# Optimization experiments

Hardware: AMD Instinct MI355X
Metric: run time of the kernel (lower is better)

## Reference

```python
import jax, jax.numpy as jnp
import numpy as np

B, S, D = 8, 4096, 256
H, DK, DV = 8, 32, 32


def _layer_norm(x, g, b, eps=1e-6):
    mu = jnp.mean(x, axis=-1, keepdims=True)
    var = jnp.mean(jnp.square(x - mu), axis=-1, keepdims=True)
    return (x - mu) * jax.lax.rsqrt(var + eps) * g + b


def setup_inputs() -> dict:
    key = jax.random.key(0)
    ks = jax.random.split(key, 16)
    std = 1.0 / np.sqrt(D)
    p = lambda k, shp: (jax.random.normal(k, shp, jnp.float32) * std)
    return {
        "h": jax.random.normal(ks[0], (B, S, D), jnp.float32),
        "e": jax.random.normal(ks[1], (B, S, D), jnp.float32),
        "s": jax.random.normal(ks[2], (B, D), jnp.float32),
        "sat_wq": p(ks[3], (D, H * DK)), "sat_wk": p(ks[4], (D, H * DK)),
        "sat_wv": p(ks[5], (D, H * DV)), "sat_wo": p(ks[6], (H * DV, D)),
        "sat_g": jnp.ones((D,), jnp.float32), "sat_b": jnp.zeros((D,), jnp.float32),
        "rel_wq": p(ks[7], (D, H * DK)), "rel_wk": p(ks[8], (D, H * DK)),
        "rel_wv": p(ks[9], (D, H * DV)), "rel_wo": p(ks[10], (H * DV, D)),
        "rel_g": jnp.ones((D,), jnp.float32), "rel_b": jnp.zeros((D,), jnp.float32),
    }


def reference(h, e, s, sat_wq, sat_wk, sat_wv, sat_wo, sat_g, sat_b,
              rel_wq, rel_wk, rel_wv, rel_wo, rel_g, rel_b):
    b, sl, d = h.shape
    scale = 1.0 / np.sqrt(DK)

    # ---- build 5-token context: [left, self, right, entity, relay] ----
    hp = jnp.pad(h, ((0, 0), (1, 1), (0, 0)))  # zeros at both ends
    s_exp = jnp.broadcast_to(s[:, None, :], (b, sl, d))
    ctx = jnp.stack([hp[:, :sl], h, hp[:, 2:], e, s_exp], axis=2)  # [B,S,5,D]

    # ---- satellite attention: 1 query vs 5-token context per position ----
    q = (h @ sat_wq).reshape(b, sl, H, DK)
    k = (ctx @ sat_wk).reshape(b, sl, 5, H, DK)
    v = (ctx @ sat_wv).reshape(b, sl, 5, H, DV)
    attn = jax.nn.softmax(jnp.einsum('bshd,bschd->bshc', q, k) * scale, axis=-1)
    o = jnp.einsum('bshc,bschd->bshd', attn, v).reshape(b, sl, H * DV) @ sat_wo
    h_out = _layer_norm(o + h, sat_g, sat_b)  # [B,S,D]

    # ---- relay attention: relay query vs [s; h_out] ----
    s_h = jnp.concatenate([s[:, None, :], h_out], axis=1)  # [B,S+1,D]
    qr = (s @ rel_wq).reshape(b, H, DK)
    kr = (s_h @ rel_wk).reshape(b, sl + 1, H, DK)
    vr = (s_h @ rel_wv).reshape(b, sl + 1, H, DV)
    attn_r = jax.nn.softmax(jnp.einsum('bhd,bkhd->bhk', qr, kr) * scale, axis=-1)
    orl = jnp.einsum('bhk,bkhd->bhd', attn_r, vr).reshape(b, H * DV) @ rel_wo
    s_out = _layer_norm(orl + s, rel_g, rel_b)  # [B,D]

    return (h_out, s_out)
```

## Files before the change

### kernel.cpp

```cpp
#include <hip/hip_runtime.h>
#include <hip/hip_bf16.h>

typedef unsigned short ushort_t;
typedef unsigned int uint_t;
typedef __attribute__((ext_vector_type(8))) short bf16x8;
typedef __attribute__((ext_vector_type(4))) float f32x4;

#define NB 8
#define NS 4096
#define ND 256
#define NH 8
#define NDK 32
#define NBS (NB*NS)
#define NK  (NS+1)
#define CH  513
#define NCH 8
static const size_t PBUF = (size_t)NB*(NS+1)*ND;
static const size_t HSZ  = (size_t)NBS*ND;

__device__ __forceinline__ ushort_t f2b(float x){
  union { __hip_bfloat16 b; ushort_t u; } cv; cv.b = __float2bfloat16(x); return cv.u;
}
__device__ __forceinline__ float b2f(ushort_t u){
  union { uint_t u; float f; } cv; cv.u = ((uint_t)u) << 16; return cv.f;
}
__device__ __forceinline__ void gload16(const ushort_t* g, ushort_t* l){
  __builtin_amdgcn_global_load_lds(
      (const __attribute__((address_space(1))) void*)g,
      (__attribute__((address_space(3))) void*)l, 16, 0, 0);
}
__device__ __forceinline__ uint4 packbf16x8(float4 a, float4 b){
  uint4 p;
  p.x = f2b(a.x) | ((uint_t)f2b(a.y)<<16);
  p.y = f2b(a.z) | ((uint_t)f2b(a.w)<<16);
  p.z = f2b(b.x) | ((uint_t)f2b(b.y)<<16);
  p.w = f2b(b.z) | ((uint_t)f2b(b.w)<<16);
  return p;
}

__device__ __forceinline__ float bsum256(float v){
  __shared__ float tmp[4];
  #pragma unroll
  for (int o=32;o>0;o>>=1) v += __shfl_down(v,o);
  if ((threadIdx.x & 63)==0) tmp[threadIdx.x>>6] = v;
  __syncthreads();
  float r = tmp[0]+tmp[1]+tmp[2]+tmp[3];
  __syncthreads();
  return r;
}

__global__ __launch_bounds__(256) void prep(
    const float* __restrict__ w0, const float* __restrict__ w1, const float* __restrict__ w2,
    const float* __restrict__ w3, const float* __restrict__ w4, const float* __restrict__ w5,
    ushort_t* __restrict__ WtAll,
    const float* __restrict__ s,
    const float* __restrict__ rwq,
    ushort_t* __restrict__ ksb, ushort_t* __restrict__ vsb,
    float* __restrict__ qr, ushort_t* __restrict__ krv)
{
  __shared__ float sh[64*68];
  const int blk = blockIdx.x;
  const int tid = threadIdx.x;
  if (blk < 96){
    const int z = blk >> 4, xy = blk & 15;
    const float* W = (z==0)?w0:(z==1)?w1:(z==2)?w2:(z==3)?w3:(z==4)?w4:w5;
    ushort_t* Wt = WtAll + (size_t)z*65536;
    float (*t)[68] = (float(*)[68])sh;
    const int k0 = (xy>>2)*64, n0 = (xy&3)*64;
    const int tr = tid>>4, tc4 = (tid&15)*4;
    #pragma unroll
    for (int i=0;i<4;i++){
      int r = tr + i*16;
      float4 v = *(const float4*)&W[(size_t)(k0+r)*ND + n0 + tc4];
      t[r][tc4]=v.x; t[r][tc4+1]=v.y; t[r][tc4+2]=v.z; t[r][tc4+3]=v.w;
    }
    __syncthreads();
    #pragma unroll
    for (int i=0;i<4;i++){
      int n = tr + i*16;
      uint_t q0 = f2b(t[tc4+0][n]) | ((uint_t)f2b(t[tc4+1][n])<<16);
      uint_t q1 = f2b(t[tc4+2][n]) | ((uint_t)f2b(t[tc4+3][n])<<16);
      *(uint2*)&Wt[(size_t)(n0+n)*ND + k0 + tc4] = make_uint2(q0,q1);
    }
  } else {
    const int rem = blk - 96;
    const int b = rem & 7, which = rem >> 3;
    const float* W = (which==0)?w1:(which==1)?w2:(which==2)?rwq:(which==3)?w4:w5;
    float* a = sh;
    a[tid] = s[(size_t)b*ND + tid];
    __syncthreads();
    float acc = 0.f;
    #pragma unroll 8
    for (int d=0; d<ND; d++)
      acc = fmaf(a[d], W[(size_t)d*ND + tid], acc);
    switch (which){
      case 0: ksb[(size_t)b*ND + tid] = f2b(acc); break;
      case 1: vsb[(size_t)b*ND + tid] = f2b(acc); break;
      case 2: qr[(size_t)b*ND + tid] = acc; break;
      case 3: krv[(size_t)b*NK*512 + tid] = f2b(acc); break;
      default: krv[(size_t)b*NK*512 + 256 + tid] = f2b(acc); break;
    }
  }
}

__global__ __launch_bounds__(512) void gemm_qkve(const float* __restrict__ hA,
    const float* __restrict__ eA, const ushort_t* __restrict__ Wt,
    ushort_t* __restrict__ hQKV, ushort_t* __restrict__ eKV)
{
  __shared__ __align__(16) ushort_t Ap[64][256];
  __shared__ __align__(16) ushort_t Bs[3][128][64];
  const int blk = blockIdx.x;
  const bool isH = blk < 512;
  const float* A = isH ? hA : eA;
  const ushort_t* Wb = isH ? Wt : (Wt + 65536);
  ushort_t* Y = isH ? hQKV : eKV;
  const int ldn  = isH ? 768 : 512;
  const int ncol = isH ? 6 : 4;
  const int row0 = (blk & 511) * 64;
  const int tid = threadIdx.x;
  const int lane = tid & 63;
  const int wave = tid >> 6;
  const int wr  = (wave>>2)*32;
  const int wcw = (wave&3)*32;
  const int l15 = lane & 15, lg = lane >> 4;
  const int lr8 = lane >> 3;
  const int ls  = (lane & 7) ^ lr8;

  #pragma unroll
  for (int i=0;i<4;i++){
    int sgi = tid + i*512;
    int r   = sgi >> 5;
    int c8  = (sgi & 31) * 8;
    const float* ga = A + (size_t)(row0 + r)*ND + c8;
    float4 a0 = *(const float4*)ga, a1 = *(const float4*)(ga+4);
    int byte = r*512 + ((c8*2) ^ ((r&7)<<4));
    *(uint4*)((char*)&Ap[0][0] + byte) = packbf16x8(a0,a1);
  }
  asm volatile("s_waitcnt lgkmcnt(0)" ::: "memory");

  const ushort_t* Bbase = Wb + (size_t)(wave*16 + lr8)*ND + ls*8;
  #define STAGEB(ct, kt, bb) do{ \
    const ushort_t* bp = Bbase + (size_t)(ct)*128*ND + (kt)*64; \
    gload16(bp,                &Bs[bb][wave*16][0]); \
    gload16(bp + (size_t)8*ND, &Bs[bb][wave*16+8][0]); \
  }while(0)

  const f32x4 vzero = {0.f,0.f,0.f,0.f};
  f32x4 acc[2][2] = {};
  const int total = ncol*4;
  STAGEB(0, 0, 0);
  int bcur = 0, bnxt = 1;
  for (int s = 0; s < total; ++s){
    const int kt = s & 3;
    const bool more = (s+1 < total);
    if (more) STAGEB((s+1)>>2, (s+1)&3, bnxt);
    if (more) asm volatile("s_waitcnt vmcnt(2)" ::: "memory");
    else      asm volatile("s_waitcnt vmcnt(0)" ::: "memory");
    __builtin_amdgcn_s_barrier();
    __builtin_amdgcn_sched_barrier(0);
    #pragma unroll
    for (int ks=0; ks<2; ks++){
      bf16x8 af[2], bfr[2];
      #pragma unroll
      for (int mi=0;mi<2;mi++){
        int ra  = wr + mi*16 + l15;
        int cb2 = kt*128 + ks*64 + lg*16;
        af[mi] = *(const bf16x8*)((const char*)&Ap[0][0] + ra*512 + (cb2 ^ ((ra&7)<<4)));
      }
      #pragma unroll
      for (int ni=0;ni<2;ni++){
        int rb = wcw + ni*16 + l15;
        int cb = (ks<<6) + (lg<<4);
        bfr[ni] = *(const bf16x8*)((const char*)&Bs[bcur][0][0] + rb*128 + (cb ^ ((rb&7)<<4)));
      }
      #pragma unroll
      for (int mi=0;mi<2;mi++)
        #pragma unroll
        for (int ni=0;ni<2;ni++)
          acc[mi][ni] = __builtin_amdgcn_mfma_f32_16x16x32_bf16(af[mi], bfr[ni], acc[mi][ni], 0,0,0);
    }
    bcur = bnxt; bnxt = (bnxt == 2) ? 0 : bnxt + 1;
    if (kt == 3){
      const int col0 = (s >> 2) * 128;
      #pragma unroll
      for (int mi=0;mi<2;mi++)
        #pragma unroll
        for (int r=0;r<4;r++){
          size_t orow = (size_t)(row0 + wr + mi*16 + lg*4 + r);
          #pragma unroll
          for (int ni=0;ni<2;ni++)
            Y[orow*(size_t)ldn + col0 + wcw + ni*16 + l15] = f2b(acc[mi][ni][r]);
        }
      #pragma unroll
      for (int mi=0;mi<2;mi++)
        #pragma unroll
        for (int ni=0;ni<2;ni++)
          acc[mi][ni] = vzero;
    }
  }
  #undef STAGEB
}

__global__ __launch_bounds__(512) void oproj_krv(const ushort_t* __restrict__ A,
    const ushort_t* __restrict__ Wto, const ushort_t* __restrict__ WtKRV,
    const float* __restrict__ hres,
    const float* __restrict__ g, const float* __restrict__ bta,
    float* __restrict__ outf, ushort_t* __restrict__ krv)
{
  __shared__ __align__(16) ushort_t Pool[2][128][64];
  __shared__ __align__(16) ushort_t Ap[64][256];
  __shared__ float rs[64][4], rq[64][4];
  __shared__ float gl[ND], bl[ND];
  const int tid  = threadIdx.x;
  const int row0 = blockIdx.x*64;
  const int lane = tid & 63;
  const int wave = tid >> 6;
  const int wr = (wave>>2)*32;
  const int wc = (wave&3)*64;
  const int wcw = (wave&3)*32;
  const int l15 = lane & 15, lg = lane >> 4;
  const int lr8 = lane >> 3;
  const int ls  = (lane & 7) ^ lr8;

  if (tid < ND){ gl[tid] = g[tid]; bl[tid] = bta[tid]; }

  ushort_t (*As)[64][64] = (ushort_t(*)[64][64])&Pool[0][0][0];
  const ushort_t* Asrc = A + (size_t)(row0 + wave*8 + lr8)*ND + ls*8;

  f32x4 acc[2][4] = {};

  #define STAGE3(t, bb) gload16(Asrc + (t)*64, &As[bb][wave*8][0])
  #define COMPUTE3(t, bb) do{ \
    _Pragma("unroll") \
    for (int ks=0; ks<2; ks++){ \
      bf16x8 af[2], bfr[4]; \
      _Pragma("unroll") \
      for (int mi=0;mi<2;mi++){ \
        int ra = wr + mi*16 + l15; int cb = (ks<<6) + (lg<<4); \
        af[mi] = *(const bf16x8*)((const char*)&As[bb][0][0] + ra*128 + (cb ^ ((ra&7)<<4))); \
      } \
      _Pragma("unroll") \
      for (int ni=0;ni<4;ni++) \
        bfr[ni] = *(const bf16x8*)&Wto[(size_t)(wc + ni*16 + l15)*ND + (t)*64 + ks*32 + lg*8]; \
      _Pragma("unroll") \
      for (int mi=0;mi<2;mi++) \
        _Pragma("unroll") \
        for (int ni=0;ni<4;ni++) \
          acc[mi][ni] = __builtin_amdgcn_mfma_f32_16x16x32_bf16(af[mi], bfr[ni], acc[mi][ni], 0,0,0); \
    } \
  }while(0)

  STAGE3(0, 0);
  __syncthreads();
  STAGE3(1, 1); COMPUTE3(0, 0); __syncthreads();
  STAGE3(2, 0); COMPUTE3(1, 1); __syncthreads();
  STAGE3(3, 1); COMPUTE3(2, 0); __syncthreads();
  COMPUTE3(3, 1);
  #undef STAGE3
  #undef COMPUTE3

  #pragma unroll
  for (int mi=0;mi<2;mi++)
    #pragma unroll
    for (int rr=0;rr<4;rr++){
      size_t rowb = (size_t)(row0 + wr + mi*16 + lg*4 + rr)*ND;
      #pragma unroll
      for (int ni=0;ni<4;ni++)
        acc[mi][ni][rr] += hres[rowb + wc + ni*16 + l15];
    }

  #pragma unroll
  for (int mi=0;mi<2;mi++)
    #pragma unroll
    for (int rr=0;rr<4;rr++){
      float sv = 0.f, qv = 0.f;
      #pragma unroll
      for (int ni=0;ni<4;ni++){ float x = acc[mi][ni][rr]; sv += x; qv += x*x; }
      #pragma unroll
      for (int o=1;o<16;o<<=1){ sv += __shfl_xor(sv,o); qv += __shfl_xor(qv,o); }
      if (l15 == 0){
        int rl = wr + mi*16 + lg*4 + rr;
        rs[rl][wave&3] = sv; rq[rl][wave&3] = qv;
      }
    }
  __syncthreads();

  #pragma unroll
  for (int mi=0;mi<2;mi++)
    #pragma unroll
    for (int rr=0;rr<4;rr++){
      int rl = wr + mi*16 + lg*4 + rr;
      float sm = rs[rl][0] + rs[rl][1] + rs[rl][2] + rs[rl][3];
      float sq = rq[rl][0] + rq[rl][1] + rq[rl][2] + rq[rl][3];
      float mu = sm * (1.0f/ND);
      float var = sq * (1.0f/ND) - mu*mu;
      float rstd = rsqrtf(var + 1e-6f);
      size_t rowb = (size_t)(row0 + rl)*ND;
      #pragma unroll
      for (int ni=0;ni<4;ni++){
        int col = wc + ni*16 + l15;
        float yv = (acc[mi][ni][rr] - mu)*rstd*gl[col] + bl[col];
        outf[rowb + col] = yv;
        int byte = rl*512 + ((col*2) ^ ((rl&7)<<4));
        *(ushort_t*)((char*)&Ap[0][0] + byte) = f2b(yv);
      }
    }

  const ushort_t* Bbase = WtKRV + (size_t)(wave*16 + lr8)*ND + ls*8;
  #define STAGEB(ct, kt, bb) do{ \
    const ushort_t* bp = Bbase + (size_t)(ct)*128*ND + (kt)*64; \
    gload16(bp,                &Pool[bb][wave*16][0]); \
    gload16(bp + (size_t)8*ND, &Pool[bb][wave*16+8][0]); \
  }while(0)

  const f32x4 vzero = {0.f,0.f,0.f,0.f};
  f32x4 acc2[2][2] = {};
  STAGEB(0,0,0);
  __syncthreads();
  int buf = 0;
  for (int s = 0; s < 16; ++s){
    const int kt = s & 3;
    if (s+1 < 16) STAGEB((s+1)>>2, (s+1)&3, buf^1);
    #pragma unroll
    for (int ks=0; ks<2; ks++){
      bf16x8 af[2], bfr[2];
      #pragma unroll
      for (int mi=0;mi<2;mi++){
        int ra  = wr + mi*16 + l15;
        int cb2 = kt*128 + ks*64 + lg*16;
        af[mi] = *(const bf16x8*)((const char*)&Ap[0][0] + ra*512 + (cb2 ^ ((ra&7)<<4)));
      }
      #pragma unroll
      for (int ni=0;ni<2;ni++){
        int rb = wcw + ni*16 + l15;
        int cb = (ks<<6) + (lg<<4);
        bfr[ni] = *(const bf16x8*)((const char*)&Pool[buf][0][0] + rb*128 + (cb ^ ((rb&7)<<4)));
      }
      #pragma unroll
      for (int mi=0;mi<2;mi++)
        #pragma unroll
        for (int ni=0;ni<2;ni++)
          acc2[mi][ni] = __builtin_amdgcn_mfma_f32_16x16x32_bf16(af[mi], bfr[ni], acc2[mi][ni], 0,0,0);
    }
    __syncthreads();
    buf ^= 1;
    if (kt == 3){
      const int col0 = (s >> 2) * 128;
      #pragma unroll
      for (int mi=0;mi<2;mi++)
        #pragma unroll
        for (int r=0;r<4;r++){
          int row = row0 + wr + mi*16 + lg*4 + r;
          size_t orow = (size_t)(row>>12)*NK + 1 + (row&4095);
          #pragma unroll
          for (int ni=0;ni<2;ni++)
            krv[orow*512 + col0 + wcw + ni*16 + l15] = f2b(acc2[mi][ni][r]);
        }
      #pragma unroll
      for (int mi=0;mi<2;mi++)
        #pragma unroll
        for (int ni=0;ni<2;ni++)
          acc2[mi][ni] = vzero;
    }
  }
  #undef STAGEB
}

__device__ __forceinline__ void load8(float* d, const ushort_t* p){
  bf16x8 v = *(const bf16x8*)p;
  #pragma unroll
  for (int i=0;i<8;i++) d[i] = b2f((ushort_t)v[i]);
}
__device__ __forceinline__ void zero8(float* d){
  #pragma unroll
  for (int i=0;i<8;i++) d[i] = 0.f;
}
__global__ __launch_bounds__(256) void sat_attn4(const ushort_t* __restrict__ HQ,
    const ushort_t* __restrict__ EKV,
    const ushort_t* __restrict__ KS, const ushort_t* __restrict__ VS,
    ushort_t* __restrict__ O)
{
  const int tid = threadIdx.x;
  const int l  = tid & 3;
  const int g  = tid >> 2;
  const int hh = g & 7;
  const int pi = g >> 3;
  const int pos = blockIdx.x*8 + pi;
  const int b = pos >> 12, t = pos & 4095;
  const int co = hh*NDK + l*8;
  const float scale = 0.17677669529663687f;

  const size_t rq = (size_t)pos*768;
  const size_t re = (size_t)pos*512;
  float q[8], k0[8], k1[8], k2[8], k3[8], k4[8];
  load8(q,  HQ + rq + co);
  load8(k1, HQ + rq + 256 + co);
  load8(k3, EKV + re + co);
  load8(k4, KS + (size_t)b*ND + co);
  if (t > 0)    load8(k0, HQ + rq - 768 + 256 + co);
  else          zero8(k0);
  if (t < NS-1) load8(k2, HQ + rq + 768 + 256 + co);
  else          zero8(k2);

  float s0=0.f,s1=0.f,s2=0.f,s3=0.f,s4=0.f;
  #pragma unroll
  for (int i=0;i<8;i++){
    s0 = fmaf(q[i],k0[i],s0); s1 = fmaf(q[i],k1[i],s1); s2 = fmaf(q[i],k2[i],s2);
    s3 = fmaf(q[i],k3[i],s3); s4 = fmaf(q[i],k4[i],s4);
  }
  #pragma unroll
  for (int mm=1; mm<4; mm<<=1){
    s0 += __shfl_xor(s0,mm); s1 += __shfl_xor(s1,mm); s2 += __shfl_xor(s2,mm);
    s3 += __shfl_xor(s3,mm); s4 += __shfl_xor(s4,mm);
  }
  s0*=scale; s1*=scale; s2*=scale; s3*=scale; s4*=scale;
  float m = fmaxf(fmaxf(fmaxf(s0,s1),fmaxf(s2,s3)),s4);
  float p0=expf(s0-m), p1=expf(s1-m), p2=expf(s2-m), p3=expf(s3-m), p4=expf(s4-m);
  float inv = 1.0f/(p0+p1+p2+p3+p4);

  float v0[8], v1[8], v2[8], v3[8], v4[8];
  load8(v1, HQ + rq + 512 + co);
  load8(v3, EKV + re + 256 + co);
  load8(v4, VS + (size_t)b*ND + co);
  if (t > 0)    load8(v0, HQ + rq - 768 + 512 + co);
  else          zero8(v0);
  if (t < NS-1) load8(v2, HQ + rq + 768 + 512 + co);
  else          zero8(v2);

  float o[8];
  #pragma unroll
  for (int i=0;i<8;i++)
    o[i] = (p0*v0[i] + p1*v1[i] + p2*v2[i] + p3*v3[i] + p4*v4[i]) * inv;
  uint4 pk;
  pk.x = f2b(o[0])|((uint_t)f2b(o[1])<<16);
  pk.y = f2b(o[2])|((uint_t)f2b(o[3])<<16);
  pk.z = f2b(o[4])|((uint_t)f2b(o[5])<<16);
  pk.w = f2b(o[6])|((uint_t)f2b(o[7])<<16);
  *(uint4*)&O[(size_t)pos*ND + co] = pk;
}

__global__ __launch_bounds__(256) void rel_part(const float* __restrict__ QR,
    const ushort_t* __restrict__ KRV,
    float* __restrict__ pO, float* __restrict__ pM, float* __restrict__ pL)
{
  const int bh = blockIdx.x;
  const int b = bh >> 3, h = bh & 7;
  const int c = blockIdx.y;
  const int k0 = c*CH;
  const int kn = min(NK, k0+CH) - k0;
  const int tid = threadIdx.x;
  __shared__ float sc[CH];
  __shared__ float qs[NDK];
  __shared__ float red[8][NDK];
  __shared__ float tmp[4];
  if (tid < NDK) qs[tid] = QR[(size_t)b*ND + h*NDK + tid];
  __syncthreads();
  const float scale = 0.17677669529663687f;
  for (int kk=tid; kk<kn; kk+=256){
    const ushort_t* kp = KRV + ((size_t)b*NK + k0 + kk)*512 + h*NDK;
    float sdot = 0.f;
    #pragma unroll
    for (int w=0; w<4; w++){
      bf16x8 kv = *(const bf16x8*)(kp + w*8);
      #pragma unroll
      for (int i=0;i<8;i++) sdot = fmaf(qs[w*8+i], b2f((ushort_t)kv[i]), sdot);
    }
    sc[kk] = sdot * scale;
  }
  __syncthreads();
  float lm = -1e30f;
  for (int kk=tid; kk<kn; kk+=256) lm = fmaxf(lm, sc[kk]);
  #pragma unroll
  for (int o=32;o>0;o>>=1) lm = fmaxf(lm, __shfl_down(lm,o));
  if ((tid & 63)==0) tmp[tid>>6] = lm;
  __syncthreads();
  float m = fmaxf(fmaxf(tmp[0],tmp[1]),fmaxf(tmp[2],tmp[3]));
  __syncthreads();
  float ls = 0.f;
  for (int kk=tid; kk<kn; kk+=256){ float p = expf(sc[kk]-m); sc[kk] = p; ls += p; }
  #pragma unroll
  for (int o=32;o>0;o>>=1) ls += __shfl_down(ls,o);
  if ((tid & 63)==0) tmp[tid>>6] = ls;
  __syncthreads();
  float lsum = tmp[0]+tmp[1]+tmp[2]+tmp[3];
  int grp = tid>>5, d = tid&31;
  float acc = 0.f;
  for (int kk=grp; kk<kn; kk+=8)
    acc = fmaf(sc[kk], b2f(KRV[((size_t)b*NK + k0 + kk)*512 + 256 + h*NDK + d]), acc);
  red[grp][d] = acc;
  __syncthreads();
  if (grp == 0){
    float tot = 0.f;
    #pragma unroll
    for (int i=0;i<8;i++) tot += red[i][d];
    pO[((size_t)bh*NCH + c)*NDK + d] = tot;
    if (d == 0){ pM[bh*NCH + c] = m; pL[bh*NCH + c] = lsum; }
  }
}

__global__ __launch_bounds__(256) void rel_tail(const float* __restrict__ pO,
    const float* __restrict__ pM, const float* __restrict__ pL,
    const float* __restrict__ WO, const float* __restrict__ Sv,
    const float* __restrict__ g, const float* __restrict__ bta,
    float* __restrict__ out)
{
  const int b = blockIdx.x, j = threadIdx.x;
  __shared__ float ol[ND];
  {
    const int h = j >> 5, d = j & 31;
    const int bh = b*NH + h;
    float m = -1e30f;
    #pragma unroll
    for (int c=0;c<NCH;c++) m = fmaxf(m, pM[bh*NCH + c]);
    float o = 0.f, l = 0.f;
    #pragma unroll
    for (int c=0;c<NCH;c++){
      float w = expf(pM[bh*NCH + c] - m);
      o = fmaf(pO[((size_t)bh*NCH + c)*NDK + d], w, o);
      l = fmaf(pL[bh*NCH + c], w, l);
    }
    ol[j] = o / l;
  }
  __syncthreads();
  float x = 0.f;
  for (int d=0; d<ND; d++) x = fmaf(ol[d], WO[(size_t)d*ND + j], x);
  x += Sv[(size_t)b*ND + j];
  float mu = bsum256(x) * (1.0f/ND);
  float dd = x - mu;
  float var = bsum256(dd*dd) * (1.0f/ND);
  out[(size_t)NBS*ND + (size_t)b*ND + j] = dd * rsqrtf(var + 1e-6f) * g[j] + bta[j];
}

extern "C" void kernel_launch(void* const* d_in, const int* in_sizes, int n_in,
                              void* d_out, int out_size, void* d_ws, size_t ws_size,
                              hipStream_t stream)
{
  const float* h      = (const float*)d_in[0];
  const float* e      = (const float*)d_in[1];
  const float* s      = (const float*)d_in[2];
  const float* sat_wq = (const float*)d_in[3];
  const float* sat_wk = (const float*)d_in[4];
  const float* sat_wv = (const float*)d_in[5];
  const float* sat_wo = (const float*)d_in[6];
  const float* sat_g  = (const float*)d_in[7];
  const float* sat_b  = (const float*)d_in[8];
  const float* rel_wq = (const float*)d_in[9];
  const float* rel_wk = (const float*)d_in[10];
  const float* rel_wv = (const float*)d_in[11];
  const float* rel_wo = (const float*)d_in[12];
  const float* rel_g  = (const float*)d_in[13];
  const float* rel_b  = (const float*)d_in[14];
  float* out = (float*)d_out;

  float* ws = (float*)d_ws;
  ushort_t* hQKV = (ushort_t*)ws;
  ushort_t* eKV  = (ushort_t*)(ws + 2*PBUF);
  ushort_t* krv  = (ushort_t*)(ws + 4*PBUF);
  ushort_t* satO = (ushort_t*)(ws + 5*PBUF);
  ushort_t* Wt   = satO + HSZ;
  float* smalls  = (float*)(Wt + 6*65536);
  ushort_t* ksb = (ushort_t*)smalls;
  ushort_t* vsb = ksb + 2048;
  float* qr  = smalls + 4096;
  float* pO  = smalls + 8192;
  float* pM  = pO + (size_t)NB*NH*NCH*NDK;
  float* pL  = pM + NB*NH*NCH;

  dim3 gb(256);

  prep<<<136, gb, 0, stream>>>(sat_wq, sat_wk, sat_wv, sat_wo, rel_wk, rel_wv, Wt,
                               s, rel_wq, ksb, vsb, qr, krv);

  gemm_qkve<<<1024, dim3(512), 0, stream>>>(h, e, Wt, hQKV, eKV);

  sat_attn4<<<NBS/8, gb, 0, stream>>>(hQKV, eKV, ksb, vsb, satO);

  oproj_krv<<<NBS/64, dim3(512), 0, stream>>>(satO, Wt + 3*65536, Wt + 4*65536,
                                              h, sat_g, sat_b, out, krv);

  rel_part<<<dim3(NB*NH, NCH), gb, 0, stream>>>(qr, krv, pO, pM, pL);

  rel_tail<<<NB, gb, 0, stream>>>(pO, pM, pL, rel_wo, s, rel_g, rel_b, out);
}
```

Measured before the change: 151.6 us.

## Fuse satellite attention into the output-projection kernel via shared memory

The separate satellite-attention kernel is removed. Its per-position softmax over the 5-token context now runs at the start of the o-projection kernel, which writes each 64-row attention tile straight into a swizzled shared-memory buffer that feeds the MFMA GEMM. This drops one kernel launch and the global write and re-read of the bf16 attention output. In exchange the GEMM loses its double-buffered staging, and each block has to finish its attention phase before any matrix math starts.

```diff
diff --git a/kernel.cpp b/kernel.cpp
--- a/kernel.cpp
+++ b/kernel.cpp
@@ -201,7 +201,9 @@
   #undef STAGEB
 }
 
-__global__ __launch_bounds__(512) void oproj_krv(const ushort_t* __restrict__ A,
+__global__ __launch_bounds__(512) void sat_oproj_krv(
+    const ushort_t* __restrict__ HQ, const ushort_t* __restrict__ EKV,
+    const ushort_t* __restrict__ KS, const ushort_t* __restrict__ VS,
     const ushort_t* __restrict__ Wto, const ushort_t* __restrict__ WtKRV,
     const float* __restrict__ hres,
     const float* __restrict__ g, const float* __restrict__ bta,
@@ -224,40 +226,95 @@
 
   if (tid < ND){ gl[tid] = g[tid]; bl[tid] = bta[tid]; }
 
-  ushort_t (*As)[64][64] = (ushort_t(*)[64][64])&Pool[0][0][0];
-  const ushort_t* Asrc = A + (size_t)(row0 + wave*8 + lr8)*ND + ls*8;
+  {
+    const int l4 = tid & 3;
+    const int grp = tid >> 2;
+    const int hh = grp & 7;
+    const int prow = grp >> 3;
+    const float scale = 0.17677669529663687f;
+    #pragma unroll
+    for (int it=0; it<4; ++it){
+      const int pl = it*16 + prow;
+      const int pos = row0 + pl;
+      const int bb = pos >> 12, tt = pos & 4095;
+      const int co = hh*NDK + l4*8;
+      const size_t rq_ = (size_t)pos*768;
+      const size_t re_ = (size_t)pos*512;
+      float q[8], k0[8], k1[8], k2[8], k3[8], k4[8];
+      {
+        bf16x8 v;
+        v = *(const bf16x8*)(HQ + rq_ + co);              for(int i=0;i<8;i++) q[i]=b2f((ushort_t)v[i]);
+        v = *(const bf16x8*)(HQ + rq_ + 256 + co);        for(int i=0;i<8;i++) k1[i]=b2f((ushort_t)v[i]);
+        v = *(const bf16x8*)(EKV + re_ + co);             for(int i=0;i<8;i++) k3[i]=b2f((ushort_t)v[i]);
+        v = *(const bf16x8*)(KS + (size_t)bb*ND + co);    for(int i=0;i<8;i++) k4[i]=b2f((ushort_t)v[i]);
+        if (tt > 0){ v = *(const bf16x8*)(HQ + rq_ - 768 + 256 + co); for(int i=0;i<8;i++) k0[i]=b2f((ushort_t)v[i]); }
+        else        for(int i=0;i<8;i++) k0[i]=0.f;
+        if (tt < NS-1){ v = *(const bf16x8*)(HQ + rq_ + 768 + 256 + co); for(int i=0;i<8;i++) k2[i]=b2f((ushort_t)v[i]); }
+        else        for(int i=0;i<8;i++) k2[i]=0.f;
+      }
+      float s0=0.f,s1=0.f,s2=0.f,s3=0.f,s4=0.f;
+      #pragma unroll
+      for (int i=0;i<8;i++){
+        s0 = fmaf(q[i],k0[i],s0); s1 = fmaf(q[i],k1[i],s1); s2 = fmaf(q[i],k2[i],s2);
+        s3 = fmaf(q[i],k3[i],s3); s4 = fmaf(q[i],k4[i],s4);
+      }
+      #pragma unroll
+      for (int mm=1; mm<4; mm<<=1){
+        s0 += __shfl_xor(s0,mm); s1 += __shfl_xor(s1,mm); s2 += __shfl_xor(s2,mm);
+        s3 += __shfl_xor(s3,mm); s4 += __shfl_xor(s4,mm);
+      }
+      s0*=scale; s1*=scale; s2*=scale; s3*=scale; s4*=scale;
+      float m = fmaxf(fmaxf(fmaxf(s0,s1),fmaxf(s2,s3)),s4);
+      float p0=expf(s0-m), p1=expf(s1-m), p2=expf(s2-m), p3=expf(s3-m), p4=expf(s4-m);
+      float inv = 1.0f/(p0+p1+p2+p3+p4);
+      float v0[8], v1[8], v2[8], v3[8], v4[8];
+      {
+        bf16x8 v;
+        v = *(const bf16x8*)(HQ + rq_ + 512 + co);        for(int i=0;i<8;i++) v1[i]=b2f((ushort_t)v[i]);
+        v = *(const bf16x8*)(EKV + re_ + 256 + co);       for(int i=0;i<8;i++) v3[i]=b2f((ushort_t)v[i]);
+        v = *(const bf16x8*)(VS + (size_t)bb*ND + co);    for(int i=0;i<8;i++) v4[i]=b2f((ushort_t)v[i]);
+        if (tt > 0){ v = *(const bf16x8*)(HQ + rq_ - 768 + 512 + co); for(int i=0;i<8;i++) v0[i]=b2f((ushort_t)v[i]); }
+        else        for(int i=0;i<8;i++) v0[i]=0.f;
+        if (tt < NS-1){ v = *(const bf16x8*)(HQ + rq_ + 768 + 512 + co); for(int i=0;i<8;i++) v2[i]=b2f((ushort_t)v[i]); }
+        else        for(int i=0;i<8;i++) v2[i]=0.f;
+      }
+      float o[8];
+      #pragma unroll
+      for (int i=0;i<8;i++)
+        o[i] = (p0*v0[i] + p1*v1[i] + p2*v2[i] + p3*v3[i] + p4*v4[i]) * inv;
+      uint4 pk;
+      pk.x = f2b(o[0])|((uint_t)f2b(o[1])<<16);
+      pk.y = f2b(o[2])|((uint_t)f2b(o[3])<<16);
+      pk.z = f2b(o[4])|((uint_t)f2b(o[5])<<16);
+      pk.w = f2b(o[6])|((uint_t)f2b(o[7])<<16);
+      int byte = pl*512 + ((co*2) ^ ((pl&7)<<4));
+      *(uint4*)((char*)&Ap[0][0] + byte) = pk;
+    }
+  }
+  __syncthreads();
 
   f32x4 acc[2][4] = {};
-
-  #define STAGE3(t, bb) gload16(Asrc + (t)*64, &As[bb][wave*8][0])
-  #define COMPUTE3(t, bb) do{ \
-    _Pragma("unroll") \
-    for (int ks=0; ks<2; ks++){ \
-      bf16x8 af[2], bfr[4]; \
-      _Pragma("unroll") \
-      for (int mi=0;mi<2;mi++){ \
-        int ra = wr + mi*16 + l15; int cb = (ks<<6) + (lg<<4); \
-        af[mi] = *(const bf16x8*)((const char*)&As[bb][0][0] + ra*128 + (cb ^ ((ra&7)<<4))); \
-      } \
-      _Pragma("unroll") \
-      for (int ni=0;ni<4;ni++) \
-        bfr[ni] = *(const bf16x8*)&Wto[(size_t)(wc + ni*16 + l15)*ND + (t)*64 + ks*32 + lg*8]; \
-      _Pragma("unroll") \
-      for (int mi=0;mi<2;mi++) \
-        _Pragma("unroll") \
-        for (int ni=0;ni<4;ni++) \
-          acc[mi][ni] = __builtin_amdgcn_mfma_f32_16x16x32_bf16(af[mi], bfr[ni], acc[mi][ni], 0,0,0); \
-    } \
-  }while(0)
-
-  STAGE3(0, 0);
-  __syncthreads();
-  STAGE3(1, 1); COMPUTE3(0, 0); __syncthreads();
-  STAGE3(2, 0); COMPUTE3(1, 1); __syncthreads();
-  STAGE3(3, 1); COMPUTE3(2, 0); __syncthreads();
-  COMPUTE3(3, 1);
-  #undef STAGE3
-  #undef COMPUTE3
+  #pragma unroll
+  for (int t=0;t<4;t++){
+    #pragma unroll
+    for (int ks=0; ks<2; ks++){
+      bf16x8 af[2], bfr[4];
+      #pragma unroll
+      for (int mi=0;mi<2;mi++){
+        int ra  = wr + mi*16 + l15;
+        int cb2 = t*128 + ks*64 + lg*16;
+        af[mi] = *(const bf16x8*)((const char*)&Ap[0][0] + ra*512 + (cb2 ^ ((ra&7)<<4)));
+      }
+      #pragma unroll
+      for (int ni=0;ni<4;ni++)
+        bfr[ni] = *(const bf16x8*)&Wto[(size_t)(wc + ni*16 + l15)*ND + t*64 + ks*32 + lg*8];
+      #pragma unroll
+      for (int mi=0;mi<2;mi++)
+        #pragma unroll
+        for (int ni=0;ni<4;ni++)
+          acc[mi][ni] = __builtin_amdgcn_mfma_f32_16x16x32_bf16(af[mi], bfr[ni], acc[mi][ni], 0,0,0);
+    }
+  }
 
   #pragma unroll
   for (int mi=0;mi<2;mi++)
@@ -364,79 +421,6 @@
     }
   }
   #undef STAGEB
-}
-
-__device__ __forceinline__ void load8(float* d, const ushort_t* p){
-  bf16x8 v = *(const bf16x8*)p;
-  #pragma unroll
-  for (int i=0;i<8;i++) d[i] = b2f((ushort_t)v[i]);
-}
-__device__ __forceinline__ void zero8(float* d){
-  #pragma unroll
-  for (int i=0;i<8;i++) d[i] = 0.f;
-}
-__global__ __launch_bounds__(256) void sat_attn4(const ushort_t* __restrict__ HQ,
-    const ushort_t* __restrict__ EKV,
-    const ushort_t* __restrict__ KS, const ushort_t* __restrict__ VS,
-    ushort_t* __restrict__ O)
-{
-  const int tid = threadIdx.x;
-  const int l  = tid & 3;
-  const int g  = tid >> 2;
-  const int hh = g & 7;
-  const int pi = g >> 3;
-  const int pos = blockIdx.x*8 + pi;
-  const int b = pos >> 12, t = pos & 4095;
-  const int co = hh*NDK + l*8;
-  const float scale = 0.17677669529663687f;
-
-  const size_t rq = (size_t)pos*768;
-  const size_t re = (size_t)pos*512;
-  float q[8], k0[8], k1[8], k2[8], k3[8], k4[8];
-  load8(q,  HQ + rq + co);
-  load8(k1, HQ + rq + 256 + co);
-  load8(k3, EKV + re + co);
-  load8(k4, KS + (size_t)b*ND + co);
-  if (t > 0)    load8(k0, HQ + rq - 768 + 256 + co);
-  else          zero8(k0);
-  if (t < NS-1) load8(k2, HQ + rq + 768 + 256 + co);
-  else          zero8(k2);
-
-  float s0=0.f,s1=0.f,s2=0.f,s3=0.f,s4=0.f;
-  #pragma unroll
-  for (int i=0;i<8;i++){
-    s0 = fmaf(q[i],k0[i],s0); s1 = fmaf(q[i],k1[i],s1); s2 = fmaf(q[i],k2[i],s2);
-    s3 = fmaf(q[i],k3[i],s3); s4 = fmaf(q[i],k4[i],s4);
-  }
-  #pragma unroll
-  for (int mm=1; mm<4; mm<<=1){
-    s0 += __shfl_xor(s0,mm); s1 += __shfl_xor(s1,mm); s2 += __shfl_xor(s2,mm);
-    s3 += __shfl_xor(s3,mm); s4 += __shfl_xor(s4,mm);
-  }
-  s0*=scale; s1*=scale; s2*=scale; s3*=scale; s4*=scale;
-  float m = fmaxf(fmaxf(fmaxf(s0,s1),fmaxf(s2,s3)),s4);
-  float p0=expf(s0-m), p1=expf(s1-m), p2=expf(s2-m), p3=expf(s3-m), p4=expf(s4-m);
-  float inv = 1.0f/(p0+p1+p2+p3+p4);
-
-  float v0[8], v1[8], v2[8], v3[8], v4[8];
-  load8(v1, HQ + rq + 512 + co);
-  load8(v3, EKV + re + 256 + co);
-  load8(v4, VS + (size_t)b*ND + co);
-  if (t > 0)    load8(v0, HQ + rq - 768 + 512 + co);
-  else          zero8(v0);
-  if (t < NS-1) load8(v2, HQ + rq + 768 + 512 + co);
-  else          zero8(v2);
-
-  float o[8];
-  #pragma unroll
-  for (int i=0;i<8;i++)
-    o[i] = (p0*v0[i] + p1*v1[i] + p2*v2[i] + p3*v3[i] + p4*v4[i]) * inv;
-  uint4 pk;
-  pk.x = f2b(o[0])|((uint_t)f2b(o[1])<<16);
-  pk.y = f2b(o[2])|((uint_t)f2b(o[3])<<16);
-  pk.z = f2b(o[4])|((uint_t)f2b(o[5])<<16);
-  pk.w = f2b(o[6])|((uint_t)f2b(o[7])<<16);
-  *(uint4*)&O[(size_t)pos*ND + co] = pk;
 }
 
 __global__ __launch_bounds__(256) void rel_part(const float* __restrict__ QR,
@@ -556,8 +540,7 @@
   ushort_t* hQKV = (ushort_t*)ws;
   ushort_t* eKV  = (ushort_t*)(ws + 2*PBUF);
   ushort_t* krv  = (ushort_t*)(ws + 4*PBUF);
-  ushort_t* satO = (ushort_t*)(ws + 5*PBUF);
-  ushort_t* Wt   = satO + HSZ;
+  ushort_t* Wt   = (ushort_t*)(ws + 5*PBUF);
   float* smalls  = (float*)(Wt + 6*65536);
   ushort_t* ksb = (ushort_t*)smalls;
   ushort_t* vsb = ksb + 2048;
@@ -573,10 +556,9 @@
 
   gemm_qkve<<<1024, dim3(512), 0, stream>>>(h, e, Wt, hQKV, eKV);
 
-  sat_attn4<<<NBS/8, gb, 0, stream>>>(hQKV, eKV, ksb, vsb, satO);
-
-  oproj_krv<<<NBS/64, dim3(512), 0, stream>>>(satO, Wt + 3*65536, Wt + 4*65536,
-                                              h, sat_g, sat_b, out, krv);
+  sat_oproj_krv<<<NBS/64, dim3(512), 0, stream>>>(hQKV, eKV, ksb, vsb,
+                                                  Wt + 3*65536, Wt + 4*65536,
+                                                  h, sat_g, sat_b, out, krv);
 
   rel_part<<<dim3(NB*NH, NCH), gb, 0, stream>>>(qr, krv, pO, pM, pL);
 
```

Result: faster. 144.4 us, median of 3 (-4.8%).
